# Performance work log

Hardware: AMD Instinct MI355X
Metric: run time of the kernel (lower is better)

Reference implementation:

```python
import jax, jax.numpy as jnp
import numpy as np

TEMPERATURE = 0.5
EPS = 1e-12  # torch F.normalize eps


def _l2_normalize(x, axis):
    norm = jnp.sqrt(jnp.sum(x * x, axis=axis, keepdims=True))
    return x / jnp.maximum(norm, EPS)


def setup_inputs() -> dict:
    key = jax.random.key(0)
    k1, k2 = jax.random.split(key)
    B, C, H, W = 16, 256, 64, 64
    teacher_vectors = jax.random.normal(k1, (B, C, H, W), dtype=jnp.float32)
    student_vectors = jax.random.normal(k2, (B, C, H, W), dtype=jnp.float32)
    return {"teacher_vectors": teacher_vectors, "student_vectors": student_vectors}


def reference(teacher_vectors, student_vectors):
    B, C, H, W = teacher_vectors.shape
    T = TEMPERATURE
    # first normalize over class dim (dim=1), as in the torch module
    t = _l2_normalize(teacher_vectors, axis=1)
    s = _l2_normalize(student_vectors, axis=1)
    # per-sample: view (C, H*W) and row-normalize
    t = _l2_normalize(t.reshape(B, C, H * W), axis=2)  # [B, C, D]
    s = _l2_normalize(s.reshape(B, C, H * W), axis=2)  # [B, C, D]
    # batched similarity: student @ teacher^T per sample -> [B, C, C]
    sim = jnp.einsum('bcd,bed->bce', s, t)
    pos = jnp.diagonal(sim, axis1=1, axis2=2)  # [B, C]
    # -log(exp(pos/T) / sum(exp(sim/T))) = -pos/T + logsumexp(sim/T)
    lse = jax.nn.logsumexp(sim.reshape(B, C * C) / T, axis=1)  # [B]
    per_sample = jnp.mean(-pos / T + lse[:, None], axis=1)  # mean over classes
    return jnp.mean(per_sample)
```

## Files before the change

kernel.cpp:

```cpp
#include <hip/hip_runtime.h>
#include <hip/hip_bf16.h>

typedef short bf16x8 __attribute__((ext_vector_type(8)));
typedef float f32x4 __attribute__((ext_vector_type(4)));
typedef unsigned short u16x8 __attribute__((ext_vector_type(8)));

#define GLOAD(gp, lp)                                                          \
    __builtin_amdgcn_global_load_lds(                                          \
        (const __attribute__((address_space(1))) void*)(gp),                   \
        (__attribute__((address_space(3))) void*)(lp), 16, 0, 0)

#define PIN8(v)                                                                \
    asm volatile("" ::"v"((v)[0]), "v"((v)[1]), "v"((v)[2]), "v"((v)[3]),      \
                 "v"((v)[4]), "v"((v)[5]), "v"((v)[6]), "v"((v)[7]))

static constexpr int kB = 16;
static constexpr int kC = 256;
static constexpr int kHW = 4096;

static constexpr int OFF_INVC_T = 0;
static constexpr int OFF_INVC_S = 65536;
static constexpr int OFF_INVD_T = 131072;
static constexpr int OFF_INVD_S = 135168;
static constexpr int OFF_EXPS   = 139264;
static constexpr int OFF_POSS   = 139280;
static constexpr size_t OFF_U_BYTES = 139296ull * 4ull;
static constexpr size_t U_ELEMS = (size_t)kB * kC * kHW;
static constexpr size_t OFF_PSIM = 139296ull + 16777216ull;

__device__ __forceinline__ unsigned short f2bf(float f) {
    __hip_bfloat16 h = __float2bfloat16(f);
    return __builtin_bit_cast(unsigned short, h);
}
__device__ __forceinline__ float bf2f(unsigned short h) {
    union { unsigned int i; float f; } u;
    u.i = ((unsigned int)h) << 16;
    return u.f;
}

__global__ __launch_bounds__(256) void cast_colnorm_k(const float* __restrict__ ten,
                                                      const float* __restrict__ stu,
                                                      float* __restrict__ ws)
{
    int tid = threadIdx.x;
    int t   = blockIdx.x;
    if (t == 0 && tid < 32) ws[OFF_EXPS + tid] = 0.0f;

    int hwc = t & 3;
    int cs  = (t >> 2) & 31;
    int b   = (t >> 7) & 15;
    int ts  = t >> 11;
    const float* src = ts ? stu : ten;

    int hw0 = hwc * 1024 + tid * 4;
    size_t base = (size_t)b * (kC * kHW) + (size_t)cs * 8 * kHW + hw0;
    const float* p = src + base;
    unsigned short* xb = (unsigned short*)((char*)ws + OFF_U_BYTES)
                       + (size_t)ts * U_ELEMS + base;

    f32x4 v[8];
#pragma unroll
    for (int j = 0; j < 8; ++j)
        v[j] = *(const f32x4*)(p + (size_t)j * kHW);
    PIN8(v);

    f32x4 acc = {0.0f, 0.0f, 0.0f, 0.0f};
#pragma unroll
    for (int j = 0; j < 8; ++j) {
        acc[0] += v[j][0] * v[j][0];
        acc[1] += v[j][1] * v[j][1];
        acc[2] += v[j][2] * v[j][2];
        acc[3] += v[j][3] * v[j][3];
        ushort4 o;
        o.x = f2bf(v[j][0]); o.y = f2bf(v[j][1]);
        o.z = f2bf(v[j][2]); o.w = f2bf(v[j][3]);
        *(ushort4*)(xb + (size_t)j * kHW) = o;
    }

    float* part = ws + OFF_PSIM + ((size_t)(ts * 32 + cs) << 16) + b * kHW + hw0;
    *(f32x4*)part = acc;
}

__global__ __launch_bounds__(256) void invc_fin_k(float* __restrict__ ws)
{
    int g0  = (blockIdx.x * 256 + threadIdx.x) * 4;
    int ts  = g0 >> 16;
    int pos = g0 & 65535;

    const float* part = ws + OFF_PSIM + ((size_t)(ts * 32) << 16) + pos;
    float4 s = {0.0f, 0.0f, 0.0f, 0.0f};
#pragma unroll
    for (int q = 0; q < 4; ++q) {
        f32x4 v[8];
#pragma unroll
        for (int cs = 0; cs < 8; ++cs)
            v[cs] = *(const f32x4*)(part + ((size_t)(q * 8 + cs) << 16));
        PIN8(v);
#pragma unroll
        for (int cs = 0; cs < 8; ++cs) {
            s.x += v[cs][0]; s.y += v[cs][1]; s.z += v[cs][2]; s.w += v[cs][3];
        }
    }
    float4 o;
    o.x = 1.0f / fmaxf(sqrtf(s.x), 1e-12f);
    o.y = 1.0f / fmaxf(sqrtf(s.y), 1e-12f);
    o.z = 1.0f / fmaxf(sqrtf(s.z), 1e-12f);
    o.w = 1.0f / fmaxf(sqrtf(s.w), 1e-12f);
    *(float4*)(ws + (ts ? OFF_INVC_S : OFF_INVC_T) + pos) = o;
}

__global__ __launch_bounds__(256) void rowscale_k(float* __restrict__ ws)
{
    int tid = threadIdx.x;
    int bc  = blockIdx.x;
    int b   = bc >> 8;
    bool isT = (blockIdx.y == 0);
    unsigned short* u = (unsigned short*)((char*)ws + OFF_U_BYTES)
                      + (isT ? 0 : U_ELEMS) + (size_t)bc * kHW;
    const float* crow = ws + (isT ? OFF_INVC_T : OFF_INVC_S) + b * kHW;
    float* invD       = ws + (isT ? OFF_INVD_T : OFF_INVD_S);

    int e0 = tid * 16;
    u16x8 xa = *(const u16x8*)(u + e0);
    u16x8 xb2 = *(const u16x8*)(u + e0 + 8);
    f32x4 c[4];
#pragma unroll
    for (int q = 0; q < 4; ++q)
        c[q] = *(const f32x4*)(crow + e0 + q * 4);

    float ss = 0.0f;
    u16x8 oa, ob;
#pragma unroll
    for (int j = 0; j < 8; ++j) {
        float pa = bf2f(xa[j]) * c[j >> 2][j & 3];
        ss += pa * pa;
        oa[j] = f2bf(pa);
    }
#pragma unroll
    for (int j = 0; j < 8; ++j) {
        float pb = bf2f(xb2[j]) * c[2 + (j >> 2)][j & 3];
        ss += pb * pb;
        ob[j] = f2bf(pb);
    }
    *(u16x8*)(u + e0)     = oa;
    *(u16x8*)(u + e0 + 8) = ob;

#pragma unroll
    for (int o = 32; o; o >>= 1) ss += __shfl_down(ss, o);
    __shared__ float red[4];
    if ((tid & 63) == 0) red[tid >> 6] = ss;
    __syncthreads();
    if (tid == 0)
        invD[bc] = 1.0f / fmaxf(sqrtf(red[0] + red[1] + red[2] + red[3]), 1e-12f);
}

__global__ __launch_bounds__(256) void gemm_part_k(float* __restrict__ ws,
                                                   int kIters)
{
    const unsigned short* uT = (const unsigned short*)((const char*)ws + OFF_U_BYTES);
    const unsigned short* uS = uT + U_ELEMS;
    float* psim = ws + OFF_PSIM;

    __shared__ __align__(16) unsigned short As[2][4096];
    __shared__ __align__(16) unsigned short Bs[2][4096];

    int tid = threadIdx.x;
    int bid = blockIdx.x;
    int cpx = gridDim.x >> 3;
    int w   = (bid & 7) * cpx + (bid >> 3);
    int tile = w & 15;
    int g    = w >> 4;
    int b    = g & 15;
    int kz   = g >> 4;
    int tr   = tile >> 2, tc = tile & 3;
    int lane = tid & 63, wid = tid >> 6;
    int wr   = wid >> 1, wc = wid & 1;

    int k0base = kz * (kIters * 64);

    int D0  = tid * 16;
    int r0s = D0 >> 7;
    int c0s = ((D0 & 127) ^ ((r0s & 7) << 4)) >> 1;
    int D1  = 4096 + tid * 16;
    int r1s = D1 >> 7;
    int c1s = ((D1 & 127) ^ ((r1s & 7) << 4)) >> 1;

    const unsigned short* gA = uS + ((size_t)(b * kC + tr * 64) << 12) + k0base;
    const unsigned short* gB = uT + ((size_t)(b * kC + tc * 64) << 12) + k0base;

    f32x4 acc[2][2] = {};

    GLOAD(gA + ((size_t)r0s << 12) + c0s, (char*)As[0] + D0);
    GLOAD(gA + ((size_t)r1s << 12) + c1s, (char*)As[0] + D1);
    GLOAD(gB + ((size_t)r0s << 12) + c0s, (char*)Bs[0] + D0);
    GLOAD(gB + ((size_t)r1s << 12) + c1s, (char*)Bs[0] + D1);
    __syncthreads();

    int cur = 0;
    for (int it = 0; it < kIters; ++it) {
        if (it + 1 < kIters) {
            int k0 = (it + 1) * 64;
            GLOAD(gA + ((size_t)r0s << 12) + k0 + c0s, (char*)As[cur ^ 1] + D0);
            GLOAD(gA + ((size_t)r1s << 12) + k0 + c1s, (char*)As[cur ^ 1] + D1);
            GLOAD(gB + ((size_t)r0s << 12) + k0 + c0s, (char*)Bs[cur ^ 1] + D0);
            GLOAD(gB + ((size_t)r1s << 12) + k0 + c1s, (char*)Bs[cur ^ 1] + D1);
        }
        const char* Ab = (const char*)As[cur];
        const char* Bb = (const char*)Bs[cur];
#pragma unroll
        for (int ks = 0; ks < 2; ++ks) {
            bf16x8 av[2], bv[2];
            int kb = ks * 64 + (lane >> 4) * 16;
#pragma unroll
            for (int f = 0; f < 2; ++f) {
                int row = wr * 32 + f * 16 + (lane & 15);
                av[f] = *(const bf16x8*)(Ab + (row << 7) + (kb ^ ((row & 7) << 4)));
                int col = wc * 32 + f * 16 + (lane & 15);
                bv[f] = *(const bf16x8*)(Bb + (col << 7) + (kb ^ ((col & 7) << 4)));
            }
#pragma unroll
            for (int fr = 0; fr < 2; ++fr)
#pragma unroll
                for (int fc = 0; fc < 2; ++fc)
                    acc[fr][fc] = __builtin_amdgcn_mfma_f32_16x16x32_bf16(
                        av[fr], bv[fc], acc[fr][fc], 0, 0, 0);
        }
        __syncthreads();
        cur ^= 1;
    }

    float* pt = psim + ((size_t)(kz * 16 + b) << 16);
#pragma unroll
    for (int fr = 0; fr < 2; ++fr)
#pragma unroll
        for (int fc = 0; fc < 2; ++fc) {
            int col = tc * 64 + wc * 32 + fc * 16 + (lane & 15);
#pragma unroll
            for (int j = 0; j < 4; ++j) {
                int row = tr * 64 + wr * 32 + fr * 16 + (lane >> 4) * 4 + j;
                pt[row * 256 + col] = acc[fr][fc][j];
            }
        }
}

__global__ __launch_bounds__(256) void reduce_k(float* __restrict__ ws, int KS)
{
    const float* psim  = ws + OFF_PSIM;
    const float* invDt = ws + OFF_INVD_T;
    const float* invDs = ws + OFF_INVD_S;

    int b     = blockIdx.x >> 6;
    int local = ((blockIdx.x & 63) << 10) + threadIdx.x * 4;
    int row   = local >> 8;
    int col   = local & 255;

    float4 s = {0.0f, 0.0f, 0.0f, 0.0f};
    for (int ks = 0; ks < KS; ++ks) {
        float4 v = *(const float4*)(psim + (((size_t)(ks * 16 + b)) << 16) + local);
        s.x += v.x; s.y += v.y; s.z += v.z; s.w += v.w;
    }
    float  ds = invDs[b * 256 + row];
    float4 dt = *(const float4*)(invDt + b * 256 + col);
    float v0 = s.x * ds * dt.x;
    float v1 = s.y * ds * dt.y;
    float v2 = s.z * ds * dt.z;
    float v3 = s.w * ds * dt.w;

    float eAcc = __expf(2.0f * v0) + __expf(2.0f * v1) +
                 __expf(2.0f * v2) + __expf(2.0f * v3);
    float pAcc = 0.0f;
    if (row == col)     pAcc = v0;
    if (row == col + 1) pAcc = v1;
    if (row == col + 2) pAcc = v2;
    if (row == col + 3) pAcc = v3;

#pragma unroll
    for (int o = 32; o; o >>= 1) {
        eAcc += __shfl_down(eAcc, o);
        pAcc += __shfl_down(pAcc, o);
    }
    __shared__ float redE[4], redP[4];
    int lane = threadIdx.x & 63, wid = threadIdx.x >> 6;
    if (lane == 0) { redE[wid] = eAcc; redP[wid] = pAcc; }
    __syncthreads();
    if (threadIdx.x == 0) {
        atomicAdd(ws + OFF_EXPS + b, redE[0] + redE[1] + redE[2] + redE[3]);
        atomicAdd(ws + OFF_POSS + b, redP[0] + redP[1] + redP[2] + redP[3]);
    }
}

__global__ void finalize_k(const float* __restrict__ ws, float* __restrict__ out)
{
    if (threadIdx.x == 0) {
        const float* expSum = ws + OFF_EXPS;
        const float* posSum = ws + OFF_POSS;
        float loss = 0.0f;
        for (int b = 0; b < kB; ++b)
            loss += -2.0f * posSum[b] / (float)kC + logf(expSum[b]);
        out[0] = loss / (float)kB;
    }
}

extern "C" void kernel_launch(void* const* d_in, const int* in_sizes, int n_in,
                              void* d_out, int out_size, void* d_ws, size_t ws_size,
                              hipStream_t stream)
{
    const float* ten = (const float*)d_in[0];
    const float* stu = (const float*)d_in[1];
    float* ws  = (float*)d_ws;
    float* out = (float*)d_out;

    int KS = 4;
    {
        size_t base = OFF_PSIM * 4ull;
        if (ws_size < base + 4ull * 16 * 65536 * 4) KS = 2;
        if (ws_size < base + 2ull * 16 * 65536 * 4) KS = 1;
    }
    int kIters = (kHW / KS) / 64;

    cast_colnorm_k<<<dim3(4096), 256, 0, stream>>>(ten, stu, ws);
    invc_fin_k<<<dim3(128), 256, 0, stream>>>(ws);
    rowscale_k<<<dim3(4096, 2), 256, 0, stream>>>(ws);
    gemm_part_k<<<dim3(256 * KS), 256, 0, stream>>>(ws, kIters);
    reduce_k<<<dim3(1024), 256, 0, stream>>>(ws, KS);
    finalize_k<<<1, 64, 0, stream>>>(ws, out);
}
```

Before: 100.5 us.

## Fold teacher column scale into student operand and store GEMM partials as bf16

```diff
diff --git a/kernel.cpp b/kernel.cpp
--- a/kernel.cpp
+++ b/kernel.cpp
@@ -117,33 +117,51 @@
     bool isT = (blockIdx.y == 0);
     unsigned short* u = (unsigned short*)((char*)ws + OFF_U_BYTES)
                       + (isT ? 0 : U_ELEMS) + (size_t)bc * kHW;
-    const float* crow = ws + (isT ? OFF_INVC_T : OFF_INVC_S) + b * kHW;
+    const float* cOwn = ws + (isT ? OFF_INVC_T : OFF_INVC_S) + b * kHW;
+    const float* cT   = ws + OFF_INVC_T + b * kHW;
     float* invD       = ws + (isT ? OFF_INVD_T : OFF_INVD_S);
 
     int e0 = tid * 16;
-    u16x8 xa = *(const u16x8*)(u + e0);
+    u16x8 xa  = *(const u16x8*)(u + e0);
     u16x8 xb2 = *(const u16x8*)(u + e0 + 8);
     f32x4 c[4];
 #pragma unroll
     for (int q = 0; q < 4; ++q)
-        c[q] = *(const f32x4*)(crow + e0 + q * 4);
+        c[q] = *(const f32x4*)(cOwn + e0 + q * 4);
 
     float ss = 0.0f;
-    u16x8 oa, ob;
-#pragma unroll
-    for (int j = 0; j < 8; ++j) {
-        float pa = bf2f(xa[j]) * c[j >> 2][j & 3];
-        ss += pa * pa;
-        oa[j] = f2bf(pa);
-    }
-#pragma unroll
-    for (int j = 0; j < 8; ++j) {
-        float pb = bf2f(xb2[j]) * c[2 + (j >> 2)][j & 3];
-        ss += pb * pb;
-        ob[j] = f2bf(pb);
-    }
-    *(u16x8*)(u + e0)     = oa;
-    *(u16x8*)(u + e0 + 8) = ob;
+    if (isT) {
+#pragma unroll
+        for (int j = 0; j < 8; ++j) {
+            float pa = bf2f(xa[j]) * c[j >> 2][j & 3];
+            ss += pa * pa;
+        }
+#pragma unroll
+        for (int j = 0; j < 8; ++j) {
+            float pb = bf2f(xb2[j]) * c[2 + (j >> 2)][j & 3];
+            ss += pb * pb;
+        }
+    } else {
+        f32x4 ct[4];
+#pragma unroll
+        for (int q = 0; q < 4; ++q)
+            ct[q] = *(const f32x4*)(cT + e0 + q * 4);
+        u16x8 oa, ob;
+#pragma unroll
+        for (int j = 0; j < 8; ++j) {
+            float pa = bf2f(xa[j]) * c[j >> 2][j & 3];
+            ss += pa * pa;
+            oa[j] = f2bf(pa * ct[j >> 2][j & 3]);
+        }
+#pragma unroll
+        for (int j = 0; j < 8; ++j) {
+            float pb = bf2f(xb2[j]) * c[2 + (j >> 2)][j & 3];
+            ss += pb * pb;
+            ob[j] = f2bf(pb * ct[2 + (j >> 2)][j & 3]);
+        }
+        *(u16x8*)(u + e0)     = oa;
+        *(u16x8*)(u + e0 + 8) = ob;
+    }
 
 #pragma unroll
     for (int o = 32; o; o >>= 1) ss += __shfl_down(ss, o);
@@ -159,7 +177,6 @@
 {
     const unsigned short* uT = (const unsigned short*)((const char*)ws + OFF_U_BYTES);
     const unsigned short* uS = uT + U_ELEMS;
-    float* psim = ws + OFF_PSIM;
 
     __shared__ __align__(16) unsigned short As[2][4096];
     __shared__ __align__(16) unsigned short Bs[2][4096];
@@ -229,7 +246,8 @@
         cur ^= 1;
     }
 
-    float* pt = psim + ((size_t)(kz * 16 + b) << 16);
+    unsigned short* pt = (unsigned short*)(ws + OFF_PSIM)
+                       + ((size_t)(kz * 16 + b) << 16);
 #pragma unroll
     for (int fr = 0; fr < 2; ++fr)
 #pragma unroll
@@ -238,41 +256,40 @@
 #pragma unroll
             for (int j = 0; j < 4; ++j) {
                 int row = tr * 64 + wr * 32 + fr * 16 + (lane >> 4) * 4 + j;
-                pt[row * 256 + col] = acc[fr][fc][j];
+                pt[row * 256 + col] = f2bf(acc[fr][fc][j]);
             }
         }
 }
 
 __global__ __launch_bounds__(256) void reduce_k(float* __restrict__ ws, int KS)
 {
-    const float* psim  = ws + OFF_PSIM;
+    const unsigned short* psim = (const unsigned short*)(ws + OFF_PSIM);
     const float* invDt = ws + OFF_INVD_T;
     const float* invDs = ws + OFF_INVD_S;
 
-    int b     = blockIdx.x >> 6;
-    int local = ((blockIdx.x & 63) << 10) + threadIdx.x * 4;
+    int b     = blockIdx.x >> 5;
+    int local = ((blockIdx.x & 31) << 11) + threadIdx.x * 8;
     int row   = local >> 8;
     int col   = local & 255;
 
-    float4 s = {0.0f, 0.0f, 0.0f, 0.0f};
+    float s[8] = {0, 0, 0, 0, 0, 0, 0, 0};
     for (int ks = 0; ks < KS; ++ks) {
-        float4 v = *(const float4*)(psim + (((size_t)(ks * 16 + b)) << 16) + local);
-        s.x += v.x; s.y += v.y; s.z += v.z; s.w += v.w;
-    }
-    float  ds = invDs[b * 256 + row];
-    float4 dt = *(const float4*)(invDt + b * 256 + col);
-    float v0 = s.x * ds * dt.x;
-    float v1 = s.y * ds * dt.y;
-    float v2 = s.z * ds * dt.z;
-    float v3 = s.w * ds * dt.w;
-
-    float eAcc = __expf(2.0f * v0) + __expf(2.0f * v1) +
-                 __expf(2.0f * v2) + __expf(2.0f * v3);
-    float pAcc = 0.0f;
-    if (row == col)     pAcc = v0;
-    if (row == col + 1) pAcc = v1;
-    if (row == col + 2) pAcc = v2;
-    if (row == col + 3) pAcc = v3;
+        u16x8 v = *(const u16x8*)(psim + (((size_t)(ks * 16 + b)) << 16) + local);
+#pragma unroll
+        for (int j = 0; j < 8; ++j) s[j] += bf2f(v[j]);
+    }
+    float  ds  = invDs[b * 256 + row];
+    f32x4  dt0 = *(const f32x4*)(invDt + b * 256 + col);
+    f32x4  dt1 = *(const f32x4*)(invDt + b * 256 + col + 4);
+
+    float eAcc = 0.0f, pAcc = 0.0f;
+#pragma unroll
+    for (int j = 0; j < 8; ++j) {
+        float dt = (j < 4) ? dt0[j] : dt1[j - 4];
+        float v  = s[j] * ds * dt;
+        eAcc += __expf(2.0f * v);
+        if (row == col + j) pAcc = v;
+    }
 
 #pragma unroll
     for (int o = 32; o; o >>= 1) {
@@ -313,8 +330,7 @@
     int KS = 4;
     {
         size_t base = OFF_PSIM * 4ull;
-        if (ws_size < base + 4ull * 16 * 65536 * 4) KS = 2;
-        if (ws_size < base + 2ull * 16 * 65536 * 4) KS = 1;
+        if (ws_size < base + 16ull * 1024 * 1024) KS = 2;
     }
     int kIters = (kHW / KS) / 64;
 
@@ -322,6 +338,6 @@
     invc_fin_k<<<dim3(128), 256, 0, stream>>>(ws);
     rowscale_k<<<dim3(4096, 2), 256, 0, stream>>>(ws);
     gemm_part_k<<<dim3(256 * KS), 256, 0, stream>>>(ws, kIters);
-    reduce_k<<<dim3(1024), 256, 0, stream>>>(ws, KS);
+    reduce_k<<<dim3(512), 256, 0, stream>>>(ws, KS);
     finalize_k<<<1, 64, 0, stream>>>(ws, out);
 }
```

Measured after the change: 92.43 us. -8.0%, faster.
